# Kernel optimization log

Hardware: AMD Instinct MI355X
Metric: run time of the kernel (lower is better)

Reference implementation:

```python
import jax, jax.numpy as jnp
import numpy as np

B, L, C, H, MAX_K, TAU = 64, 512, 256, 8, 512, 1.0
N = B * L
DH = C // H


def setup_inputs() -> dict:
    key = jax.random.key(0)
    ks = jax.random.split(key, 16)
    s = 0.02
    return {
        "x": jax.random.normal(ks[0], (N, C), jnp.float32),
        "edge_index": jax.random.randint(ks[1], (2, 200000), 0, N, jnp.int64),
        "batch": jnp.repeat(jnp.arange(B, dtype=jnp.int64), L),
        "token_ratio": jax.random.uniform(ks[2], (B,), jnp.float32, 0.05, 0.95),
        # gumbel = -log(Exp(1)) matches -empty.exponential_().log()
        "gumbel": -jnp.log(jax.random.exponential(ks[3], (B, L), jnp.float32)),
        # scorer: Linear(C,C) -> ReLU -> Linear(C,1)
        "Ws1": jax.random.normal(ks[4], (C, C), jnp.float32) * s,
        "bs1": jnp.zeros((C,), jnp.float32),
        "Ws2": jax.random.normal(ks[5], (1, C), jnp.float32) * s,
        "bs2": jnp.zeros((1,), jnp.float32),
        # MultiheadAttention packed in-proj [3C, C] and out-proj [C, C]
        "Win": jax.random.normal(ks[6], (3 * C, C), jnp.float32) * s,
        "b_in": jnp.zeros((3 * C,), jnp.float32),
        "Wout": jax.random.normal(ks[7], (C, C), jnp.float32) * s,
        "bout": jnp.zeros((C,), jnp.float32),
        # MLP: Linear(C, 2C) -> ReLU -> Linear(2C, C)
        "Wm1": jax.random.normal(ks[8], (2 * C, C), jnp.float32) * s,
        "bm1": jnp.zeros((2 * C,), jnp.float32),
        "Wm2": jax.random.normal(ks[9], (C, 2 * C), jnp.float32) * s,
        "bm2": jnp.zeros((C,), jnp.float32),
    }


def reference(x, edge_index, batch, token_ratio, gumbel,
              Ws1, bs1, Ws2, bs2, Win, b_in, Wout, bout, Wm1, bm1, Wm2, bm2):
    # conv=None, norm=None, eval mode (dropout = identity), equal-length graphs
    h_dense = x.reshape(B, L, C)                                  # to_dense_batch
    real_len = L                                                  # all graphs full
    k_per = jnp.clip(jnp.ceil(token_ratio * real_len).astype(jnp.int32),
                     1, min(MAX_K, L))                            # [B]
    k_max = int(np.max(np.asarray(k_per)))                        # concrete

    # scorer -> log-softmax scores (mask is all True, no -inf fill needed)
    s1 = jax.nn.relu(h_dense @ Ws1.T + bs1)
    scores = (s1 @ Ws2.T + bs2)[..., 0]                           # [B, L]
    log_scores = jax.nn.log_softmax(scores, axis=-1)

    # gumbel top-k with straight-through one-hot mask
    y_soft = jax.nn.softmax((log_scores + gumbel) / TAU, axis=-1)
    _, idx_g = jax.lax.top_k(y_soft, k_max)                       # [B, k_max]
    bidx = jnp.arange(B)[:, None]
    y_hard = jnp.zeros_like(y_soft).at[bidx, idx_g].set(1.0)
    token_mask = y_hard + y_soft - jax.lax.stop_gradient(y_soft)  # == y_hard numerically

    # sort descending, zero tokens beyond k_per[i], scatter back to node order
    sort_idx = jnp.argsort(-jax.lax.stop_gradient(token_mask), axis=-1, stable=True)
    sorted_mask = jnp.take_along_axis(token_mask, sort_idx, axis=1)
    keep = jnp.arange(L)[None, :] < k_per[:, None]
    sorted_mask = jnp.where(keep, sorted_mask, 0.0)
    refined = jnp.zeros_like(sorted_mask).at[bidx, sort_idx].set(sorted_mask)

    # compact gather + padded self-attention
    weighted = h_dense * refined[..., None]                       # [B, L, C]
    _, topk_idx = jax.lax.top_k(jax.lax.stop_gradient(refined), k_max)
    h_compact = jnp.take_along_axis(weighted, topk_idx[..., None], axis=1)  # [B,k,C]
    compact_mask = jnp.arange(k_max)[None, :] < k_per[:, None]    # [B, k]

    qkv = h_compact @ Win.T + b_in
    q, k, v = jnp.split(qkv, 3, axis=-1)
    hd = lambda t: t.reshape(B, k_max, H, DH)
    att = jnp.einsum('bqhd,bkhd->bhqk', hd(q), hd(k)) / np.sqrt(DH)
    att = jnp.where(compact_mask[:, None, None, :], att, -jnp.inf)
    att = jax.nn.softmax(att, axis=-1)
    h_attn = jnp.einsum('bhqk,bkhd->bqhd', att, hd(v)).reshape(B, k_max, C)
    h_attn = h_attn @ Wout.T + bout

    # scatter back to dense node positions
    h_full = jnp.zeros((B, L, C), x.dtype).at[bidx, topk_idx].set(h_attn)
    h = h_full.reshape(N, C) + x
    h = h * token_ratio[batch][:, None]

    out = h  # hs == [h] since conv is None
    out = out + (jax.nn.relu(out @ Wm1.T + bm1) @ Wm2.T + bm2)
    return out
```

## Files before the change

kernel.cpp:

```cpp
#include <hip/hip_runtime.h>
#include <hip/hip_bf16.h>
#include <math.h>

#define BB 64
#define LL 512
#define CC 256
#define HH 8
#define DHH 32
#define NN (BB * LL)

typedef __attribute__((ext_vector_type(8))) short bf16x8;
typedef __attribute__((ext_vector_type(4))) float f32x4;
typedef __attribute__((ext_vector_type(4))) unsigned short us4;

#define MFMA16(a, b, c) __builtin_amdgcn_mfma_f32_16x16x32_bf16(a, b, c, 0, 0, 0)

__device__ __forceinline__ unsigned short f2bf(float f) {
  unsigned u = __builtin_bit_cast(unsigned, f);
  u += 0x7fffu + ((u >> 16) & 1u);
  return (unsigned short)(u >> 16);
}
__device__ __forceinline__ float bf2f(unsigned short h) {
  unsigned u = ((unsigned)h) << 16;
  return __builtin_bit_cast(float, u);
}

__global__ __launch_bounds__(256) void k_cvt(
    const float* __restrict__ Ws1, unsigned short* __restrict__ W1h,
    unsigned short* __restrict__ W1l, const float* __restrict__ Win,
    unsigned short* __restrict__ Winh, const float* __restrict__ Wout,
    unsigned short* __restrict__ Wouth, const float* __restrict__ Wm1,
    unsigned short* __restrict__ Wm1h, const float* __restrict__ Wm2,
    unsigned short* __restrict__ Wm2h) {
  const int NW1 = CC * CC;
  const int NWIN = 3 * CC * CC;
  const int NWM = 2 * CC * CC;
  int i = blockIdx.x * 256 + threadIdx.x;
  if (i < NW1) {
    float v = Ws1[i];
    unsigned short hb = f2bf(v);
    W1h[i] = hb;
    W1l[i] = f2bf(v - bf2f(hb));
    return;
  }
  i -= NW1;
  if (i < NWIN) { Winh[i] = f2bf(Win[i]); return; }
  i -= NWIN;
  if (i < NW1) { Wouth[i] = f2bf(Wout[i]); return; }
  i -= NW1;
  if (i < NWM) { Wm1h[i] = f2bf(Wm1[i]); return; }
  i -= NWM;
  if (i < NWM) Wm2h[i] = f2bf(Wm2[i]);
}

__global__ __launch_bounds__(512, 4) void k_scorer(
    const float* __restrict__ x, unsigned short* __restrict__ xh,
    const unsigned short* __restrict__ W1h,
    const unsigned short* __restrict__ W1l, const float* __restrict__ bs1,
    const float* __restrict__ Ws2, const float* __restrict__ bs2,
    float* __restrict__ scores) {
  __shared__ unsigned short Ah[64][264];
  __shared__ unsigned short Al[64][264];
  __shared__ float red[8][64];
  int t = threadIdx.x;
  int tok0 = blockIdx.x * 64;
  int lane = t & 63, wid = t >> 6, quad = lane >> 4, l16 = lane & 15;
  bf16x8 bhc[2], blc[2];
#pragma unroll
  for (int nt = 0; nt < 2; ++nt) {
    int n = wid * 32 + nt * 16 + l16;
    bhc[nt] = *(const bf16x8*)&W1h[(size_t)n * CC + quad * 8];
    blc[nt] = *(const bf16x8*)&W1l[(size_t)n * CC + quad * 8];
  }
  for (int idx = t; idx < 64 * 64; idx += 512) {
    int r = idx >> 6, c4 = idx & 63;
    float4 v = *(const float4*)(x + (size_t)(tok0 + r) * CC + c4 * 4);
    float vv[4] = {v.x, v.y, v.z, v.w};
    unsigned short hb[4], lb[4];
#pragma unroll
    for (int j = 0; j < 4; ++j) {
      hb[j] = f2bf(vv[j]);
      lb[j] = f2bf(vv[j] - bf2f(hb[j]));
    }
    *(us4*)&Ah[r][c4 * 4] = *(us4*)hb;
    *(us4*)&Al[r][c4 * 4] = *(us4*)lb;
    ((us4*)(xh + (size_t)(tok0 + r) * CC))[c4] = *(us4*)hb;
  }
  __syncthreads();
  f32x4 acc[4][2] = {};
  for (int k0 = 0; k0 < CC; k0 += 32) {
    bf16x8 bhn[2], bln[2];
    bool more = (k0 + 32 < CC);
    if (more) {
#pragma unroll
      for (int nt = 0; nt < 2; ++nt) {
        int n = wid * 32 + nt * 16 + l16;
        bhn[nt] = *(const bf16x8*)&W1h[(size_t)n * CC + (k0 + 32) + quad * 8];
        bln[nt] = *(const bf16x8*)&W1l[(size_t)n * CC + (k0 + 32) + quad * 8];
      }
    }
    bf16x8 ah_[4], al_[4];
#pragma unroll
    for (int rt = 0; rt < 4; ++rt) {
      ah_[rt] = *(const bf16x8*)&Ah[rt * 16 + l16][k0 + quad * 8];
      al_[rt] = *(const bf16x8*)&Al[rt * 16 + l16][k0 + quad * 8];
    }
#pragma unroll
    for (int nt = 0; nt < 2; ++nt)
#pragma unroll
      for (int rt = 0; rt < 4; ++rt) {
        acc[rt][nt] = MFMA16(ah_[rt], bhc[nt], acc[rt][nt]);
        acc[rt][nt] = MFMA16(ah_[rt], blc[nt], acc[rt][nt]);
        acc[rt][nt] = MFMA16(al_[rt], bhc[nt], acc[rt][nt]);
      }
    if (more) {
#pragma unroll
      for (int nt = 0; nt < 2; ++nt) { bhc[nt] = bhn[nt]; blc[nt] = bln[nt]; }
    }
  }
  float rs[4][4] = {};
#pragma unroll
  for (int nt = 0; nt < 2; ++nt) {
    int n = wid * 32 + nt * 16 + l16;
    float b1 = bs1[n], w2 = Ws2[n];
#pragma unroll
    for (int rt = 0; rt < 4; ++rt)
#pragma unroll
      for (int r = 0; r < 4; ++r)
        rs[rt][r] += fmaxf(acc[rt][nt][r] + b1, 0.f) * w2;
  }
#pragma unroll
  for (int o = 1; o < 16; o <<= 1)
#pragma unroll
    for (int rt = 0; rt < 4; ++rt)
#pragma unroll
      for (int r = 0; r < 4; ++r) rs[rt][r] += __shfl_xor(rs[rt][r], o);
  if (l16 == 0) {
#pragma unroll
    for (int rt = 0; rt < 4; ++rt)
#pragma unroll
      for (int r = 0; r < 4; ++r)
        red[wid][rt * 16 + quad * 4 + r] = rs[rt][r];
  }
  __syncthreads();
  if (t < 64) {
    float s = bs2[0];
#pragma unroll
    for (int w = 0; w < 8; ++w) s += red[w][t];
    scores[tok0 + t] = s;
  }
}

__global__ __launch_bounds__(512) void k_presel(
    const float* __restrict__ scores, const float* __restrict__ gumbel,
    const float* __restrict__ ratio, int* __restrict__ k_per,
    int* __restrict__ codes, int* __restrict__ row2l) {
  __shared__ float zs[LL];
  __shared__ int sel[LL];
  __shared__ float red[8];
  __shared__ int kps[64];
  int b = blockIdx.x, l = threadIdx.x;
  int lane = l & 63, wid = l >> 6;
  if (l < 64) {
    int kp_ = (int)ceilf(ratio[l] * (float)LL);
    kp_ = min(max(kp_, 1), LL);
    kps[l] = kp_;
    if (l == b) k_per[b] = kp_;
  }
  __syncthreads();
  int kp = kps[b];
  int km = 0;
#pragma unroll
  for (int j = 0; j < 64; ++j) km = max(km, kps[j]);
  float v = scores[b * LL + l];
  float m = v;
  for (int o = 32; o > 0; o >>= 1) m = fmaxf(m, __shfl_down(m, o));
  if (lane == 0) red[wid] = m;
  __syncthreads();
  m = red[0];
#pragma unroll
  for (int j = 1; j < 8; ++j) m = fmaxf(m, red[j]);
  __syncthreads();
  float e = expf(v - m);
  for (int o = 32; o > 0; o >>= 1) e += __shfl_down(e, o);
  if (lane == 0) red[wid] = e;
  __syncthreads();
  float tot = red[0];
#pragma unroll
  for (int j = 1; j < 8; ++j) tot += red[j];
  float lse = m + logf(tot);
  float zl = v - lse + gumbel[b * LL + l];
  zs[l] = zl;
  __syncthreads();
  int rank = 0;
  for (int j = 0; j < LL; ++j) {
    float zj = zs[j];
    rank += (zj > zl) || (zj == zl && j < l);
  }
  int s = (rank < km) ? 1 : 0;
  sel[l] = s;
  __syncthreads();
  int ps = 0;
  for (int j = 0; j < l; ++j) ps += sel[j];
  int kept = s && (ps < kp);
  int keptPrefix = min(ps, kp);
  int code;
  if (kept)
    code = ps;
  else if ((l - keptPrefix) < (km - kp))
    code = kp;
  else
    code = -1;
  codes[b * LL + l] = code;
  if (kept) row2l[b * LL + ps] = l;
}

__global__ __launch_bounds__(256) void k_qkv(
    const unsigned short* __restrict__ xh, const int* __restrict__ row2l,
    const int* __restrict__ k_per, const unsigned short* __restrict__ Winh,
    const float* __restrict__ b_in, unsigned short* __restrict__ qh,
    unsigned short* __restrict__ kh, unsigned short* __restrict__ vh) {
  int b = blockIdx.y;
  int kp = k_per[b];
  int rows = (kp < LL) ? kp + 1 : LL;
  int r0 = blockIdx.x * 32;
  if (r0 >= rows) return;
  __shared__ unsigned short A1[32][264];
  int t = threadIdx.x;
  for (int idx = t; idx < 32 * 64; idx += 256) {
    int r = idx >> 6, c4 = idx & 63;
    int gr = r0 + r;
    us4 v = {0, 0, 0, 0};
    if (gr < kp) {
      int l = row2l[b * LL + gr];
      v = ((const us4*)(xh + ((size_t)b * LL + l) * CC))[c4];
    }
    *(us4*)&A1[r][c4 * 4] = v;
  }
  __syncthreads();
  int lane = t & 63, wid = t >> 6, quad = lane >> 4, row16 = lane & 15;
  f32x4 acc[2][12] = {};
  for (int k0 = 0; k0 < CC; k0 += 32) {
    bf16x8 a0 = *(const bf16x8*)&A1[row16][k0 + quad * 8];
    bf16x8 a1 = *(const bf16x8*)&A1[16 + row16][k0 + quad * 8];
#pragma unroll
    for (int nt = 0; nt < 12; ++nt) {
      int n = wid * 192 + nt * 16 + row16;
      bf16x8 bfr = *(const bf16x8*)&Winh[(size_t)n * CC + k0 + quad * 8];
      acc[0][nt] = MFMA16(a0, bfr, acc[0][nt]);
      acc[1][nt] = MFMA16(a1, bfr, acc[1][nt]);
    }
  }
#pragma unroll
  for (int rt = 0; rt < 2; ++rt) {
#pragma unroll
    for (int nt = 0; nt < 12; ++nt) {
      int n = wid * 192 + nt * 16 + row16;
      int which = n >> 8, nc = n & 255;
      unsigned short* dst = (which == 0) ? qh : (which == 1) ? kh : vh;
      float bias = b_in[n];
#pragma unroll
      for (int r = 0; r < 4; ++r) {
        int row = r0 + rt * 16 + quad * 4 + r;
        if (row < rows)
          dst[((size_t)b * LL + row) * CC + nc] = f2bf(acc[rt][nt][r] + bias);
      }
    }
  }
}

__global__ __launch_bounds__(256, 4) void k_attn(
    const unsigned short* __restrict__ qh, const unsigned short* __restrict__ kh,
    const unsigned short* __restrict__ vh, const int* __restrict__ k_per,
    unsigned short* __restrict__ ah) {
  int h = blockIdx.y, b = blockIdx.z;
  int kp = k_per[b];
  int rows = (kp < LL) ? kp + 1 : LL;
  int q0 = blockIdx.x * 128;
  if (q0 >= rows) return;
  int t = threadIdx.x;
  int lane = t & 63, wid = t >> 6, quad = lane >> 4, l16 = lane & 15;

  __shared__ unsigned short Kc[128 * 40];
  __shared__ unsigned short Vt[32 * 132];
  __shared__ unsigned short Pb[4][16 * 132];

  size_t base = ((size_t)b * LL) * CC + (size_t)h * DHH;

  bf16x8 aQ[2] = {};
  float m[2][4], l[2][4];
  f32x4 o0[2] = {}, o1[2] = {};
#pragma unroll
  for (int g = 0; g < 2; ++g) {
    int myq = q0 + wid * 32 + g * 16 + l16;
    if (myq < rows)
      aQ[g] = *(const bf16x8*)(qh + base + (size_t)myq * CC + quad * 8);
#pragma unroll
    for (int r = 0; r < 4; ++r) { m[g][r] = -1e30f; l[g][r] = 0.f; }
  }
  const float scale = 0.17677669529663687f;
  int nch = (kp + 127) >> 7;
  unsigned short* Pw = Pb[wid];

  for (int c = 0; c < nch; ++c) {
    int kbase = c << 7;
    __syncthreads();
    for (int idx = t; idx < 1024; idx += 256) {
      int key = idx >> 3, c4 = idx & 7;
      int gk = kbase + key;
      us4 kv = {0, 0, 0, 0}, vv = {0, 0, 0, 0};
      if (gk < kp) {
        kv = *(const us4*)(kh + base + (size_t)gk * CC + c4 * 4);
        vv = *(const us4*)(vh + base + (size_t)gk * CC + c4 * 4);
      }
      *(us4*)&Kc[key * 40 + c4 * 4] = kv;
#pragma unroll
      for (int j = 0; j < 4; ++j) Vt[(c4 * 4 + j) * 132 + key] = vv[j];
    }
    __syncthreads();
#pragma unroll
    for (int g = 0; g < 2; ++g) {
      f32x4 s[8];
#pragma unroll
      for (int tt = 0; tt < 8; ++tt) {
        f32x4 z4 = {};
        bf16x8 bK = *(const bf16x8*)&Kc[(tt * 16 + l16) * 40 + quad * 8];
        s[tt] = MFMA16(aQ[g], bK, z4);
      }
      float cm[4] = {-1e30f, -1e30f, -1e30f, -1e30f};
#pragma unroll
      for (int tt = 0; tt < 8; ++tt) {
        float sb = (kbase + tt * 16 + l16 < kp) ? 0.f : -1e30f;
#pragma unroll
        for (int r = 0; r < 4; ++r) {
          float v = fmaf(s[tt][r], scale, sb);
          s[tt][r] = v;
          cm[r] = fmaxf(cm[r], v);
        }
      }
#pragma unroll
      for (int o = 1; o < 16; o <<= 1)
#pragma unroll
        for (int r = 0; r < 4; ++r) cm[r] = fmaxf(cm[r], __shfl_xor(cm[r], o));
      float alpha[4], cs[4] = {0.f, 0.f, 0.f, 0.f};
#pragma unroll
      for (int r = 0; r < 4; ++r) {
        float mn = fmaxf(m[g][r], cm[r]);
        alpha[r] = __expf(m[g][r] - mn);
        m[g][r] = mn;
      }
#pragma unroll
      for (int tt = 0; tt < 8; ++tt)
#pragma unroll
        for (int r = 0; r < 4; ++r) {
          float p = __expf(s[tt][r] - m[g][r]);
          s[tt][r] = p;
          cs[r] += p;
        }
#pragma unroll
      for (int o = 1; o < 16; o <<= 1)
#pragma unroll
        for (int r = 0; r < 4; ++r) cs[r] += __shfl_xor(cs[r], o);
#pragma unroll
      for (int r = 0; r < 4; ++r) {
        l[g][r] = l[g][r] * alpha[r] + cs[r];
        o0[g][r] *= alpha[r];
        o1[g][r] *= alpha[r];
      }
#pragma unroll
      for (int tt = 0; tt < 8; ++tt)
#pragma unroll
        for (int r = 0; r < 4; ++r)
          Pw[(quad * 4 + r) * 132 + tt * 16 + l16] = f2bf(s[tt][r]);
#pragma unroll
      for (int gg = 0; gg < 4; ++gg) {
        if (kbase + gg * 32 < kp) {
          bf16x8 aP = *(const bf16x8*)&Pw[l16 * 132 + gg * 32 + quad * 8];
          int koff = gg * 32 + quad * 8;
          struct U8 { us4 a, bq; };
          U8 u0, u1;
          u0.a = *(const us4*)&Vt[l16 * 132 + koff];
          u0.bq = *(const us4*)&Vt[l16 * 132 + koff + 4];
          u1.a = *(const us4*)&Vt[(16 + l16) * 132 + koff];
          u1.bq = *(const us4*)&Vt[(16 + l16) * 132 + koff + 4];
          o0[g] = MFMA16(aP, __builtin_bit_cast(bf16x8, u0), o0[g]);
          o1[g] = MFMA16(aP, __builtin_bit_cast(bf16x8, u1), o1[g]);
        }
      }
    }
  }
#pragma unroll
  for (int g = 0; g < 2; ++g)
#pragma unroll
    for (int r = 0; r < 4; ++r) {
      int q = q0 + wid * 32 + g * 16 + quad * 4 + r;
      if (q < rows) {
        float invl = 1.f / l[g][r];
        ah[base + (size_t)q * CC + l16] = f2bf(o0[g][r] * invl);
        ah[base + (size_t)q * CC + 16 + l16] = f2bf(o1[g][r] * invl);
      }
    }
}

__global__ __launch_bounds__(512, 4) void k_opmlp(
    const unsigned short* __restrict__ ah, const int* __restrict__ codes,
    const unsigned short* __restrict__ Wouth, const float* __restrict__ bout,
    const unsigned short* __restrict__ xh, const float* __restrict__ ratio,
    const unsigned short* __restrict__ Wm1h, const float* __restrict__ bm1,
    const unsigned short* __restrict__ Wm2h, const float* __restrict__ bm2,
    float* __restrict__ out) {
  int b = blockIdx.y;
  int l0 = blockIdx.x * 64;
  int t = threadIdx.x;
  __shared__ unsigned short A1[64][264];
  __shared__ unsigned short Hs[64][264];
  __shared__ int cd[64];
  if (t < 64) cd[t] = codes[b * LL + l0 + t];
  __syncthreads();
  for (int idx = t; idx < 64 * 64; idx += 512) {
    int r = idx >> 6, c4 = idx & 63;
    int c = cd[r];
    us4 v = {0, 0, 0, 0};
    if (c >= 0) v = ((const us4*)(ah + ((size_t)b * LL + c) * CC))[c4];
    *(us4*)&A1[r][c4 * 4] = v;
  }
  int lane = t & 63, wid = t >> 6, quad = lane >> 4, l16 = lane & 15;
  bf16x8 bcur[2];
#pragma unroll
  for (int nt = 0; nt < 2; ++nt)
    bcur[nt] =
        *(const bf16x8*)&Wouth[(size_t)(wid * 32 + nt * 16 + l16) * CC + quad * 8];
  unsigned short xv[4][2][4];
#pragma unroll
  for (int rt = 0; rt < 4; ++rt)
#pragma unroll
    for (int nt = 0; nt < 2; ++nt) {
      int n = wid * 32 + nt * 16 + l16;
#pragma unroll
      for (int r = 0; r < 4; ++r)
        xv[rt][nt][r] =
            xh[((size_t)b * LL + l0 + rt * 16 + quad * 4 + r) * CC + n];
    }
  __syncthreads();

  f32x4 acc[4][2] = {};
  for (int k0 = 0; k0 < CC; k0 += 32) {
    bf16x8 bnxt[2];
    bool more = (k0 + 32 < CC);
    if (more) {
#pragma unroll
      for (int nt = 0; nt < 2; ++nt)
        bnxt[nt] = *(const bf16x8*)&Wouth[(size_t)(wid * 32 + nt * 16 + l16) * CC +
                                          (k0 + 32) + quad * 8];
    }
    bf16x8 a_[4];
#pragma unroll
    for (int rt = 0; rt < 4; ++rt)
      a_[rt] = *(const bf16x8*)&A1[rt * 16 + l16][k0 + quad * 8];
#pragma unroll
    for (int nt = 0; nt < 2; ++nt)
#pragma unroll
      for (int rt = 0; rt < 4; ++rt)
        acc[rt][nt] = MFMA16(a_[rt], bcur[nt], acc[rt][nt]);
    if (more) { bcur[0] = bnxt[0]; bcur[1] = bnxt[1]; }
  }
  float rt_ratio = ratio[b];
  f32x4 acc2[4][2];
#pragma unroll
  for (int rt = 0; rt < 4; ++rt)
#pragma unroll
    for (int nt = 0; nt < 2; ++nt) {
      int n = wid * 32 + nt * 16 + l16;
      float bias = bout[n];
#pragma unroll
      for (int r = 0; r < 4; ++r) {
        int rl = rt * 16 + quad * 4 + r;
        int c = cd[rl];
        float y = (c >= 0) ? (acc[rt][nt][r] + bias) : 0.f;
        acc2[rt][nt][r] = (y + bf2f(xv[rt][nt][r])) * rt_ratio;
      }
    }
  __syncthreads();
#pragma unroll
  for (int rt = 0; rt < 4; ++rt)
#pragma unroll
    for (int nt = 0; nt < 2; ++nt) {
      int n = wid * 32 + nt * 16 + l16;
#pragma unroll
      for (int r = 0; r < 4; ++r)
        A1[rt * 16 + quad * 4 + r][n] = f2bf(acc2[rt][nt][r]);
    }
  __syncthreads();

#pragma unroll
  for (int half = 0; half < 2; ++half) {
    f32x4 acc1[4][2] = {};
    bf16x8 c1[2];
#pragma unroll
    for (int nt = 0; nt < 2; ++nt)
      c1[nt] = *(const bf16x8*)&Wm1h[(size_t)(half * 256 + wid * 32 + nt * 16 +
                                              l16) * CC + quad * 8];
    for (int k0 = 0; k0 < CC; k0 += 32) {
      bf16x8 n1[2];
      bool more = (k0 + 32 < CC);
      if (more) {
#pragma unroll
        for (int nt = 0; nt < 2; ++nt)
          n1[nt] = *(const bf16x8*)&Wm1h[(size_t)(half * 256 + wid * 32 +
                                                  nt * 16 + l16) * CC +
                                         (k0 + 32) + quad * 8];
      }
      bf16x8 a_[4];
#pragma unroll
      for (int rt = 0; rt < 4; ++rt)
        a_[rt] = *(const bf16x8*)&A1[rt * 16 + l16][k0 + quad * 8];
#pragma unroll
      for (int nt = 0; nt < 2; ++nt)
#pragma unroll
        for (int rt = 0; rt < 4; ++rt)
          acc1[rt][nt] = MFMA16(a_[rt], c1[nt], acc1[rt][nt]);
      if (more) { c1[0] = n1[0]; c1[1] = n1[1]; }
    }
    if (half == 1) __syncthreads();
#pragma unroll
    for (int rt = 0; rt < 4; ++rt)
#pragma unroll
      for (int nt = 0; nt < 2; ++nt) {
        int hc = wid * 32 + nt * 16 + l16;
        float bias = bm1[half * 256 + hc];
#pragma unroll
        for (int r = 0; r < 4; ++r) {
          float v = fmaxf(acc1[rt][nt][r] + bias, 0.f);
          Hs[rt * 16 + quad * 4 + r][hc] = f2bf(v);
        }
      }
    bf16x8 c2[2];
#pragma unroll
    for (int nt = 0; nt < 2; ++nt)
      c2[nt] = *(const bf16x8*)&Wm2h[(size_t)(wid * 32 + nt * 16 + l16) *
                                         (2 * CC) + half * 256 + quad * 8];
    __syncthreads();
    for (int k0 = 0; k0 < CC; k0 += 32) {
      bf16x8 n2[2];
      bool more = (k0 + 32 < CC);
      if (more) {
#pragma unroll
        for (int nt = 0; nt < 2; ++nt)
          n2[nt] = *(const bf16x8*)&Wm2h[(size_t)(wid * 32 + nt * 16 + l16) *
                                             (2 * CC) + half * 256 + (k0 + 32) +
                                         quad * 8];
      }
      bf16x8 h_[4];
#pragma unroll
      for (int rt = 0; rt < 4; ++rt)
        h_[rt] = *(const bf16x8*)&Hs[rt * 16 + l16][k0 + quad * 8];
#pragma unroll
      for (int nt = 0; nt < 2; ++nt)
#pragma unroll
        for (int rt = 0; rt < 4; ++rt)
          acc2[rt][nt] = MFMA16(h_[rt], c2[nt], acc2[rt][nt]);
      if (more) { c2[0] = n2[0]; c2[1] = n2[1]; }
    }
  }
#pragma unroll
  for (int rt = 0; rt < 4; ++rt)
#pragma unroll
    for (int nt = 0; nt < 2; ++nt) {
      int n = wid * 32 + nt * 16 + l16;
      float bias = bm2[n];
#pragma unroll
      for (int r = 0; r < 4; ++r) {
        int rl = rt * 16 + quad * 4 + r;
        size_t o = ((size_t)b * LL + l0 + rl) * CC + n;
        out[o] = acc2[rt][nt][r] + bias;
      }
    }
}

extern "C" void kernel_launch(void* const* d_in, const int* in_sizes, int n_in,
                              void* d_out, int out_size, void* d_ws,
                              size_t ws_size, hipStream_t stream) {
  (void)in_sizes; (void)n_in; (void)out_size; (void)ws_size;
  const float* x     = (const float*)d_in[0];
  const float* ratio = (const float*)d_in[3];
  const float* gum   = (const float*)d_in[4];
  const float* Ws1   = (const float*)d_in[5];
  const float* bs1   = (const float*)d_in[6];
  const float* Ws2   = (const float*)d_in[7];
  const float* bs2   = (const float*)d_in[8];
  const float* Win   = (const float*)d_in[9];
  const float* b_in  = (const float*)d_in[10];
  const float* Wout  = (const float*)d_in[11];
  const float* bout  = (const float*)d_in[12];
  const float* Wm1   = (const float*)d_in[13];
  const float* bm1   = (const float*)d_in[14];
  const float* Wm2   = (const float*)d_in[15];
  const float* bm2   = (const float*)d_in[16];
  float* out = (float*)d_out;

  const size_t NXC = (size_t)NN * CC;
  float* z    = (float*)d_ws;
  int* k_per  = (int*)(z + NN);
  int* codes  = k_per + 128;
  int* row2l  = codes + NN;
  unsigned short* xh    = (unsigned short*)(row2l + NN);
  unsigned short* qh    = xh + NXC;
  unsigned short* kh    = qh + NXC;
  unsigned short* vh    = kh + NXC;
  unsigned short* ahb   = vh + NXC;
  unsigned short* Winh  = ahb + NXC;
  unsigned short* Wouth = Winh + 3 * CC * CC;
  unsigned short* Wm1h  = Wouth + CC * CC;
  unsigned short* Wm2h  = Wm1h + 2 * CC * CC;
  unsigned short* W1h   = Wm2h + 2 * CC * CC;
  unsigned short* W1l   = W1h + CC * CC;

  const int cvt_total = 9 * CC * CC;
  k_cvt<<<(cvt_total + 255) / 256, 256, 0, stream>>>(
      Ws1, W1h, W1l, Win, Winh, Wout, Wouth, Wm1, Wm1h, Wm2, Wm2h);

  k_scorer<<<NN / 64, 512, 0, stream>>>(x, xh, W1h, W1l, bs1, Ws2, bs2, z);
  k_presel<<<BB, 512, 0, stream>>>(z, gum, ratio, k_per, codes, row2l);
  k_qkv<<<dim3(16, BB), 256, 0, stream>>>(xh, row2l, k_per, Winh, b_in, qh, kh, vh);
  k_attn<<<dim3(4, HH, BB), 256, 0, stream>>>(qh, kh, vh, k_per, ahb);
  k_opmlp<<<dim3(8, BB), 512, 0, stream>>>(ahb, codes, Wouth, bout, xh, ratio,
                                           Wm1h, bm1, Wm2h, bm2, out);
}
```

Measured before the change: 340.7 us.

## Prefetch next K/V chunk into registers and compute row sums via MFMA

The attention kernel now loads the next 128-key K/V chunk into registers while the current chunk is being computed, then writes it to shared memory after the barrier. The V transpose store is vectorised. The softmax denominator is now taken from an extra MFMA against a ones vector, which uses the bf16-rounded probabilities and replaces the shuffle-reduction of row sums. s_setprio is raised around the MFMA sections. This adds register pressure and one extra MFMA per tile, and the denominator changes slightly because it now sums rounded values.

```diff
diff --git a/kernel.cpp b/kernel.cpp
--- a/kernel.cpp
+++ b/kernel.cpp
@@ -288,45 +288,73 @@
   size_t base = ((size_t)b * LL) * CC + (size_t)h * DHH;
 
   bf16x8 aQ[2] = {};
-  float m[2][4], l[2][4];
-  f32x4 o0[2] = {}, o1[2] = {};
+  float m[2][4];
+  f32x4 o0[2] = {}, o1[2] = {}, o2[2] = {};
 #pragma unroll
   for (int g = 0; g < 2; ++g) {
     int myq = q0 + wid * 32 + g * 16 + l16;
     if (myq < rows)
       aQ[g] = *(const bf16x8*)(qh + base + (size_t)myq * CC + quad * 8);
 #pragma unroll
-    for (int r = 0; r < 4; ++r) { m[g][r] = -1e30f; l[g][r] = 0.f; }
-  }
+    for (int r = 0; r < 4; ++r) m[g][r] = -1e30f;
+  }
+  bf16x8 vone;
+#pragma unroll
+  for (int j = 0; j < 8; ++j) vone[j] = (short)0x3F80;
+
   const float scale = 0.17677669529663687f;
   int nch = (kp + 127) >> 7;
   unsigned short* Pw = Pb[wid];
 
+  int kK0 = t >> 2;
+  int kc8 = (t & 3) * 8;
+  int vd0 = (t & 7) * 4;
+  int vk0 = (t >> 3) * 4;
+
+  bf16x8 Kreg[2];
+  us4 Vreg[4];
+  auto LOADC = [&](int cc) {
+    int kb = cc << 7;
+#pragma unroll
+    for (int i = 0; i < 2; ++i) {
+      int gk = kb + kK0 + i * 64;
+      bf16x8 z = {};
+      if (gk < kp) z = *(const bf16x8*)(kh + base + (size_t)gk * CC + kc8);
+      Kreg[i] = z;
+    }
+#pragma unroll
+    for (int i = 0; i < 4; ++i) {
+      int gk = kb + vk0 + i;
+      us4 z4 = {0, 0, 0, 0};
+      if (gk < kp) z4 = *(const us4*)(vh + base + (size_t)gk * CC + vd0);
+      Vreg[i] = z4;
+    }
+  };
+
+  LOADC(0);
   for (int c = 0; c < nch; ++c) {
     int kbase = c << 7;
     __syncthreads();
-    for (int idx = t; idx < 1024; idx += 256) {
-      int key = idx >> 3, c4 = idx & 7;
-      int gk = kbase + key;
-      us4 kv = {0, 0, 0, 0}, vv = {0, 0, 0, 0};
-      if (gk < kp) {
-        kv = *(const us4*)(kh + base + (size_t)gk * CC + c4 * 4);
-        vv = *(const us4*)(vh + base + (size_t)gk * CC + c4 * 4);
-      }
-      *(us4*)&Kc[key * 40 + c4 * 4] = kv;
-#pragma unroll
-      for (int j = 0; j < 4; ++j) Vt[(c4 * 4 + j) * 132 + key] = vv[j];
+    *(bf16x8*)&Kc[kK0 * 40 + kc8] = Kreg[0];
+    *(bf16x8*)&Kc[(kK0 + 64) * 40 + kc8] = Kreg[1];
+#pragma unroll
+    for (int j = 0; j < 4; ++j) {
+      us4 w = {Vreg[0][j], Vreg[1][j], Vreg[2][j], Vreg[3][j]};
+      *(us4*)&Vt[(vd0 + j) * 132 + vk0] = w;
     }
     __syncthreads();
+    if (c + 1 < nch) LOADC(c + 1);
 #pragma unroll
     for (int g = 0; g < 2; ++g) {
       f32x4 s[8];
+      __builtin_amdgcn_s_setprio(1);
 #pragma unroll
       for (int tt = 0; tt < 8; ++tt) {
         f32x4 z4 = {};
         bf16x8 bK = *(const bf16x8*)&Kc[(tt * 16 + l16) * 40 + quad * 8];
         s[tt] = MFMA16(aQ[g], bK, z4);
       }
+      __builtin_amdgcn_s_setprio(0);
       float cm[4] = {-1e30f, -1e30f, -1e30f, -1e30f};
 #pragma unroll
       for (int tt = 0; tt < 8; ++tt) {
@@ -342,7 +370,7 @@
       for (int o = 1; o < 16; o <<= 1)
 #pragma unroll
         for (int r = 0; r < 4; ++r) cm[r] = fmaxf(cm[r], __shfl_xor(cm[r], o));
-      float alpha[4], cs[4] = {0.f, 0.f, 0.f, 0.f};
+      float alpha[4];
 #pragma unroll
       for (int r = 0; r < 4; ++r) {
         float mn = fmaxf(m[g][r], cm[r]);
@@ -352,26 +380,19 @@
 #pragma unroll
       for (int tt = 0; tt < 8; ++tt)
 #pragma unroll
-        for (int r = 0; r < 4; ++r) {
-          float p = __expf(s[tt][r] - m[g][r]);
-          s[tt][r] = p;
-          cs[r] += p;
-        }
-#pragma unroll
-      for (int o = 1; o < 16; o <<= 1)
-#pragma unroll
-        for (int r = 0; r < 4; ++r) cs[r] += __shfl_xor(cs[r], o);
+        for (int r = 0; r < 4; ++r) s[tt][r] = __expf(s[tt][r] - m[g][r]);
 #pragma unroll
       for (int r = 0; r < 4; ++r) {
-        l[g][r] = l[g][r] * alpha[r] + cs[r];
         o0[g][r] *= alpha[r];
         o1[g][r] *= alpha[r];
+        o2[g][r] *= alpha[r];
       }
 #pragma unroll
       for (int tt = 0; tt < 8; ++tt)
 #pragma unroll
         for (int r = 0; r < 4; ++r)
           Pw[(quad * 4 + r) * 132 + tt * 16 + l16] = f2bf(s[tt][r]);
+      __builtin_amdgcn_s_setprio(1);
 #pragma unroll
       for (int gg = 0; gg < 4; ++gg) {
         if (kbase + gg * 32 < kp) {
@@ -385,8 +406,10 @@
           u1.bq = *(const us4*)&Vt[(16 + l16) * 132 + koff + 4];
           o0[g] = MFMA16(aP, __builtin_bit_cast(bf16x8, u0), o0[g]);
           o1[g] = MFMA16(aP, __builtin_bit_cast(bf16x8, u1), o1[g]);
+          o2[g] = MFMA16(aP, vone, o2[g]);
         }
       }
+      __builtin_amdgcn_s_setprio(0);
     }
   }
 #pragma unroll
@@ -395,7 +418,7 @@
     for (int r = 0; r < 4; ++r) {
       int q = q0 + wid * 32 + g * 16 + quad * 4 + r;
       if (q < rows) {
-        float invl = 1.f / l[g][r];
+        float invl = 1.f / o2[g][r];
         ah[base + (size_t)q * CC + l16] = f2bf(o0[g][r] * invl);
         ah[base + (size_t)q * CC + 16 + l16] = f2bf(o1[g][r] * invl);
       }
```

Result: faster. 327.6 us (-3.8%).
